# Kernel optimization log

Measured on AMD Instinct MI355X. Metric: run time of the kernel, lower is better.

The kernel has to match this reference:

```python
import jax, jax.numpy as jnp
import numpy as np

D_MODEL = 1024
D_FF = 4096
NUM_EXPERTS = 8
TOP_K = 2
LN_EPS = 1e-5


def setup_inputs() -> dict:
    key = jax.random.key(0)
    ks = jax.random.split(key, 12)
    B, S, D, F, E = 4, 2048, D_MODEL, D_FF, NUM_EXPERTS
    s = 0.02
    return {
        "x": jax.random.normal(ks[0], (B, S, D), jnp.float32),
        # gating network: Linear(D, D//2) -> ReLU -> Linear(D//2, E)
        "gw1": jax.random.normal(ks[1], (D, D // 2), jnp.float32) * s,
        "gb1": jnp.zeros((D // 2,), jnp.float32),
        "gw2": jax.random.normal(ks[2], (D // 2, E), jnp.float32) * s,
        "gb2": jnp.zeros((E,), jnp.float32),
        # stacked expert FFNs: Linear(D,F) -> GELU -> Linear(F,D), then *scale + bias
        "we1": jax.random.normal(ks[3], (E, D, F), jnp.float32) * s,
        "be1": jnp.zeros((E, F), jnp.float32),
        "we2": jax.random.normal(ks[4], (E, F, D), jnp.float32) * s,
        "be2": jnp.zeros((E, D), jnp.float32),
        "escale": jnp.ones((E, D), jnp.float32),
        "ebias": jax.random.normal(ks[5], (E, D), jnp.float32) * 0.01,
        # output LayerNorm
        "gamma": jnp.ones((D,), jnp.float32),
        "beta": jnp.zeros((D,), jnp.float32),
    }


def _layernorm(x, gamma, beta):
    mu = jnp.mean(x, axis=-1, keepdims=True)
    var = jnp.mean(jnp.square(x - mu), axis=-1, keepdims=True)
    return (x - mu) * jax.lax.rsqrt(var + LN_EPS) * gamma + beta


def reference(x, gw1, gb1, gw2, gb2, we1, be1, we2, be2, escale, ebias, gamma, beta):
    B, S, D = x.shape
    xf = x.reshape(-1, D)  # [T, D]

    # ---- gating (eval mode: no noise, no dropout) ----
    gate_logits = jax.nn.relu(xf @ gw1 + gb1) @ gw2 + gb2  # [T, E]
    top_v, top_i = jax.lax.top_k(gate_logits, TOP_K)       # [T, K]
    gates = jax.nn.softmax(top_v, axis=-1)                 # [T, K]

    # load balancing loss: KL( uniform || mean softmax probs ), sum reduction
    probs = jax.nn.softmax(gate_logits, axis=-1)
    expert_probs = probs.mean(axis=0)                      # [E]
    t = 1.0 / NUM_EXPERTS
    load_loss = jnp.sum(t * (jnp.log(t) - jnp.log(expert_probs + 1e-8)))

    # ---- dense compute over ALL experts (faithful to source) ----
    h = jnp.einsum('td,edf->tef', xf, we1) + be1           # [T, E, F]
    h = jax.nn.gelu(h, approximate=False)                  # nn.GELU default = erf
    eo = jnp.einsum('tef,efd->ted', h, we2) + be2          # [T, E, D]
    eo = eo * escale + ebias                               # per-expert scale/bias

    # ---- top-k gather + weighted combine ----
    sel = jnp.take_along_axis(eo, top_i[:, :, None], axis=1)  # [T, K, D]
    out = jnp.sum(gates[:, :, None] * sel, axis=1)            # [T, D]

    y = _layernorm(x + out.reshape(B, S, D), gamma, beta)
    return y, load_loss
```

## Files before the change

### kernel.cpp

```cpp
#include <hip/hip_runtime.h>
#include <hip/hip_bf16.h>
#include <math.h>

#define T_TOK 8192
#define DM    1024
#define DFF   4096
#define NE    8
#define DH    512
#define NSLOT (T_TOK*2)
#define MAXT  136

typedef float  f32x4  __attribute__((ext_vector_type(4)));
typedef __bf16 bf16x8 __attribute__((ext_vector_type(8)));

__device__ inline ushort f2bf(float f) {
  union { float f; unsigned int u; } v; v.f = f;
  unsigned int r = (v.u + 0x7FFFu + ((v.u >> 16) & 1u)) >> 16;
  return (ushort)r;
}

__device__ inline float bf2f(ushort u) {
  union { unsigned int i; float f; } v; v.i = ((unsigned int)u) << 16; return v.f;
}

__device__ __forceinline__ float gelu_erf(float v) {
  float xx = v * 0.70710678118654752f;
  float ax = fabsf(xx);
  float t  = __builtin_amdgcn_rcpf(1.f + 0.3275911f * ax);
  float p  = t * (0.254829592f + t * (-0.284496736f + t * (1.421413741f +
             t * (-1.453152027f + t * 1.061405429f))));
  float er = 1.f - p * __expf(-ax * ax);
  er = copysignf(er, xx);
  return 0.5f * v * (1.f + er);
}

__device__ inline void gl_lds16(const void* g, void* l) {
  __builtin_amdgcn_global_load_lds(
      (const __attribute__((address_space(1))) unsigned int*)g,
      (__attribute__((address_space(3))) unsigned int*)l, 16, 0, 0);
}

__global__ void k_init(int* counts, int* fill, float* psum) {
  int i = threadIdx.x;
  if (i < NE) { counts[i] = 0; fill[i] = 0; psum[i] = 0.f; }
}

__global__ void k_cvt_x(const float* __restrict__ x, ushort* __restrict__ xh,
                        ushort* __restrict__ xl, int n4) {
  int i = blockIdx.x * blockDim.x + threadIdx.x;
  int st = gridDim.x * blockDim.x;
  for (; i < n4; i += st) {
    float4 v = ((const float4*)x)[i];
    ushort4 h, l;
    h.x = f2bf(v.x); l.x = f2bf(v.x - bf2f(h.x));
    h.y = f2bf(v.y); l.y = f2bf(v.y - bf2f(h.y));
    h.z = f2bf(v.z); l.z = f2bf(v.z - bf2f(h.z));
    h.w = f2bf(v.w); l.w = f2bf(v.w - bf2f(h.w));
    ((ushort4*)xh)[i] = h;
    ((ushort4*)xl)[i] = l;
  }
}

__global__ __launch_bounds__(256) void k_tr(const float* __restrict__ in,
                                            ushort* __restrict__ out, int R, int C) {
  __shared__ float tile[64][65];
  int e = blockIdx.z;
  in  += (size_t)e * R * C;
  out += (size_t)e * R * C;
  int r0 = blockIdx.y * 64, c0 = blockIdx.x * 64;
  int tx = threadIdx.x & 63, ty = threadIdx.x >> 6;
  for (int i = 0; i < 16; i++) {
    int r = ty + i * 4;
    tile[r][tx] = in[(size_t)(r0 + r) * C + c0 + tx];
  }
  __syncthreads();
  for (int i = 0; i < 16; i++) {
    int c = ty + i * 4;
    out[(size_t)(c0 + c) * R + r0 + tx] = f2bf(tile[tx][c]);
  }
}

__global__ __launch_bounds__(256) void k_trg(const float* __restrict__ in,
                                             ushort* __restrict__ outh,
                                             ushort* __restrict__ outl) {
  __shared__ float tile[64][65];
  int r0 = blockIdx.y * 64, c0 = blockIdx.x * 64;
  int tx = threadIdx.x & 63, ty = threadIdx.x >> 6;
  for (int i = 0; i < 16; i++) {
    int r = ty + i * 4;
    tile[r][tx] = in[(size_t)(r0 + r) * DH + c0 + tx];
  }
  __syncthreads();
  for (int i = 0; i < 16; i++) {
    int c = ty + i * 4;
    float f = tile[tx][c];
    ushort h = f2bf(f);
    outh[(size_t)(c0 + c) * DM + r0 + tx] = h;
    outl[(size_t)(c0 + c) * DM + r0 + tx] = f2bf(f - bf2f(h));
  }
}

__global__ __launch_bounds__(256) void k_gate1m(const ushort* __restrict__ xh,
                                                const ushort* __restrict__ xl,
                                                const ushort* __restrict__ w1ht,
                                                const ushort* __restrict__ w1lt,
                                                const float* __restrict__ b,
                                                float* __restrict__ g1) {
  constexpr int GX = DH / 128;
  constexpr int NWG = GX * (T_TOK / 128);
  int id = blockIdx.y * GX + blockIdx.x;
  int wg = (id & 7) * (NWG / 8) + (id >> 3);
  int m0 = (wg / GX) * 128;
  int n0 = (wg % GX) * 128;

  __shared__ ushort lds[2][16384];

  int t = threadIdx.x;
  int wave = t >> 6, lane = t & 63;
  int wr = wave >> 1, wc = wave & 1;

  int r = t >> 2;
  int csrc = (((t & 3) ^ ((t >> 3) & 3)) * 8);
  const ushort* ah0 = xh + (size_t)(m0 + r) * DM + csrc;
  const ushort* ah1 = xh + (size_t)(m0 + r + 64) * DM + csrc;
  const ushort* al0 = xl + (size_t)(m0 + r) * DM + csrc;
  const ushort* al1 = xl + (size_t)(m0 + r + 64) * DM + csrc;
  const ushort* bh0 = w1ht + (size_t)(n0 + r) * DM + csrc;
  const ushort* bh1 = w1ht + (size_t)(n0 + r + 64) * DM + csrc;
  const ushort* bl0 = w1lt + (size_t)(n0 + r) * DM + csrc;
  const ushort* bl1 = w1lt + (size_t)(n0 + r + 64) * DM + csrc;

  auto stage = [&](int b_, int k0) {
    ushort* base = lds[b_];
    gl_lds16(ah0 + k0, base + t * 8);
    gl_lds16(ah1 + k0, base + (t + 256) * 8);
    gl_lds16(al0 + k0, base + 4096 + t * 8);
    gl_lds16(al1 + k0, base + 4096 + (t + 256) * 8);
    gl_lds16(bh0 + k0, base + 8192 + t * 8);
    gl_lds16(bh1 + k0, base + 8192 + (t + 256) * 8);
    gl_lds16(bl0 + k0, base + 12288 + t * 8);
    gl_lds16(bl1 + k0, base + 12288 + (t + 256) * 8);
  };

  f32x4 acc[4][4] = {};
  int la = lane & 15;
  int kqs = (((lane >> 4) ^ ((la >> 1) & 3)) * 8);
  constexpr int NT = DM / 32;

  stage(0, 0);
  stage(1, 32);
  for (int kt = 0; kt < NT; kt++) {
    if (kt + 1 < NT) asm volatile("s_waitcnt vmcnt(8)" ::: "memory");
    else             asm volatile("s_waitcnt vmcnt(0)" ::: "memory");
    __builtin_amdgcn_s_barrier();
    const ushort* bb = lds[kt & 1];
    bf16x8 fah[4], fal[4], fbh[4], fbl[4];
#pragma unroll
    for (int m = 0; m < 4; m++) {
      int ro = (wr * 64 + m * 16 + la) * 32 + kqs;
      fah[m] = *(const bf16x8*)&bb[ro];
      fal[m] = *(const bf16x8*)&bb[4096 + ro];
    }
#pragma unroll
    for (int n = 0; n < 4; n++) {
      int ro = (wc * 64 + n * 16 + la) * 32 + kqs;
      fbh[n] = *(const bf16x8*)&bb[8192 + ro];
      fbl[n] = *(const bf16x8*)&bb[12288 + ro];
    }
    asm volatile("s_waitcnt lgkmcnt(0)" ::: "memory");
    __builtin_amdgcn_s_barrier();
    if (kt + 2 < NT) stage(kt & 1, (kt + 2) * 32);
#pragma unroll
    for (int m = 0; m < 4; m++)
#pragma unroll
      for (int n = 0; n < 4; n++)
        acc[m][n] = __builtin_amdgcn_mfma_f32_16x16x32_bf16(fah[m], fbh[n], acc[m][n], 0, 0, 0);
#pragma unroll
    for (int m = 0; m < 4; m++)
#pragma unroll
      for (int n = 0; n < 4; n++)
        acc[m][n] = __builtin_amdgcn_mfma_f32_16x16x32_bf16(fah[m], fbl[n], acc[m][n], 0, 0, 0);
#pragma unroll
    for (int m = 0; m < 4; m++)
#pragma unroll
      for (int n = 0; n < 4; n++)
        acc[m][n] = __builtin_amdgcn_mfma_f32_16x16x32_bf16(fal[m], fbh[n], acc[m][n], 0, 0, 0);
  }

#pragma unroll
  for (int m = 0; m < 4; m++) {
    int rbase = m0 + wr * 64 + m * 16 + ((lane >> 4) << 2);
#pragma unroll
    for (int n = 0; n < 4; n++) {
      int c = n0 + wc * 64 + n * 16 + la;
      float bv = b[c];
      f32x4 a = acc[m][n];
#pragma unroll
      for (int j = 0; j < 4; j++)
        g1[(size_t)(rbase + j) * DH + c] = fmaxf(a[j] + bv, 0.f);
    }
  }
}

__global__ __launch_bounds__(256) void k_gate2(const float* __restrict__ g1,
                                               const float* __restrict__ w2,
                                               const float* __restrict__ b2,
                                               float* __restrict__ logits) {
  int wave = threadIdx.x >> 6, lane = threadIdx.x & 63;
  int tok = blockIdx.x * 4 + wave;
  const float* row = &g1[(size_t)tok * DH];
  float v[8];
#pragma unroll
  for (int j = 0; j < 8; j++) v[j] = row[lane + 64 * j];
  float acc[8];
#pragma unroll
  for (int e = 0; e < NE; e++) {
    float s = 0.f;
#pragma unroll
    for (int j = 0; j < 8; j++) s += v[j] * w2[(size_t)(lane + 64 * j) * NE + e];
    acc[e] = s;
  }
  for (int off = 32; off > 0; off >>= 1)
#pragma unroll
    for (int e = 0; e < NE; e++) acc[e] += __shfl_down(acc[e], off);
  if (lane == 0)
#pragma unroll
    for (int e = 0; e < NE; e++) logits[(size_t)tok * NE + e] = acc[e] + b2[e];
}

__global__ __launch_bounds__(256) void k_route(const float* __restrict__ logits,
                                               int* __restrict__ topi,
                                               float* __restrict__ gatesw,
                                               int* __restrict__ counts,
                                               float* __restrict__ psum) {
  int t = blockIdx.x * blockDim.x + threadIdx.x;
  const float* lp = &logits[(size_t)t * NE];
  float l[8];
#pragma unroll
  for (int e = 0; e < NE; e++) l[e] = lp[e];
  int i0 = 0; float v0 = l[0];
#pragma unroll
  for (int e = 1; e < NE; e++) if (l[e] > v0) { v0 = l[e]; i0 = e; }
  int i1 = (i0 == 0) ? 1 : 0; float v1 = l[i1];
#pragma unroll
  for (int e = 0; e < NE; e++)
    if (e != i0 && l[e] > v1) { v1 = l[e]; i1 = e; }
  float g0 = 1.f / (1.f + expf(v1 - v0));
  topi[t * 2] = i0; topi[t * 2 + 1] = i1;
  gatesw[t * 2] = g0; gatesw[t * 2 + 1] = 1.f - g0;
  float p[8]; float s = 0.f;
#pragma unroll
  for (int e = 0; e < NE; e++) { p[e] = expf(l[e] - v0); s += p[e]; }
  float inv = 1.f / s;
  int lane = threadIdx.x & 63;
#pragma unroll
  for (int e = 0; e < NE; e++) {
    float pe = p[e] * inv;
    for (int off = 32; off > 0; off >>= 1) pe += __shfl_down(pe, off);
    if (lane == 0) atomicAdd(&psum[e], pe);
  }
#pragma unroll
  for (int e = 0; e < NE; e++) {
    unsigned long long m0 = __ballot(i0 == e);
    unsigned long long m1 = __ballot(i1 == e);
    if (lane == 0) {
      int c = __popcll(m0) + __popcll(m1);
      if (c) atomicAdd(&counts[e], c);
    }
  }
}

__global__ void k_scan(const int* __restrict__ counts, int* __restrict__ offsets,
                       const float* __restrict__ psum, float* __restrict__ loss_out,
                       int* __restrict__ tile_e, int* __restrict__ tile_mt) {
  if (threadIdx.x == 0) {
    int off = 0;
    for (int e = 0; e < NE; e++) { offsets[e] = off; off += counts[e]; }
    offsets[NE] = off;
    float tt = 1.f / NE, loss = 0.f;
    for (int e = 0; e < NE; e++) {
      float pe = psum[e] / (float)T_TOK;
      loss += tt * (logf(tt) - logf(pe + 1e-8f));
    }
    loss_out[0] = loss;
    int n = 0;
    for (int e = 0; e < NE; e++) {
      int rows = counts[e];
      for (int mt = 0; mt * 128 < rows; mt++) { tile_e[n] = e; tile_mt[n] = mt; n++; }
    }
    for (int i = n; i < MAXT; i++) { tile_e[i] = -1; tile_mt[i] = 0; }
  }
}

__global__ __launch_bounds__(256) void k_fill(const int* __restrict__ topi,
                                              const int* __restrict__ offsets,
                                              int* __restrict__ fill,
                                              int* __restrict__ slot_tok,
                                              int* __restrict__ tok_slot) {
  int t = blockIdx.x * blockDim.x + threadIdx.x;
  for (int k = 0; k < 2; k++) {
    int e = topi[t * 2 + k];
    int pos = offsets[e] + atomicAdd(&fill[e], 1);
    slot_tok[pos] = t;
    tok_slot[t * 2 + k] = pos;
  }
}

__global__ __launch_bounds__(256, 3) void k_egemm1(const ushort* __restrict__ xb,
                                                   const ushort* __restrict__ w1t,
                                                   const float* __restrict__ be1,
                                                   const int* __restrict__ slot_tok,
                                                   const int* __restrict__ offsets,
                                                   const int* __restrict__ tile_e,
                                                   const int* __restrict__ tile_mt,
                                                   ushort* __restrict__ H) {
  constexpr int GX = DFF / 128;
  constexpr int NWG = GX * MAXT;
  int id = blockIdx.y * GX + blockIdx.x;
  int wg = (id & 7) * (NWG / 8) + (id >> 3);
  int ty = wg / GX;
  int n0 = (wg % GX) * 128;
  int e = tile_e[ty];
  if (e < 0) return;
  int mt = tile_mt[ty];
  int beg = offsets[e], nrows = offsets[e + 1] - beg;
  const ushort* B = w1t + (size_t)e * DFF * DM;

  __shared__ ushort As[2][4096];
  __shared__ ushort Bs[2][4096];

  int t = threadIdx.x;
  int wave = t >> 6, lane = t & 63;
  int wr = wave >> 1, wc = wave & 1;

  int r_g0 = mt * 128 + (t >> 2);
  int r_g1 = r_g0 + 64;
  int tok0 = slot_tok[beg + (r_g0 < nrows ? r_g0 : 0)];
  int tok1 = slot_tok[beg + (r_g1 < nrows ? r_g1 : 0)];
  int acol = (((t & 3) ^ ((t >> 3) & 3)) * 8);
  const ushort* aptr0 = xb + (size_t)tok0 * DM + acol;
  const ushort* aptr1 = xb + (size_t)tok1 * DM + acol;
  const ushort* bptr0 = B + (size_t)(n0 + (t >> 2)) * DM + acol;
  const ushort* bptr1 = B + (size_t)(n0 + (t >> 2) + 64) * DM + acol;
  char* adst = (char*)As + t * 16;
  char* bdst = (char*)Bs + t * 16;

  auto stage = [&](int b, int k0) {
    gl_lds16(aptr0 + k0, adst + b * 8192);
    gl_lds16(aptr1 + k0, adst + b * 8192 + 4096);
    gl_lds16(bptr0 + k0, bdst + b * 8192);
    gl_lds16(bptr1 + k0, bdst + b * 8192 + 4096);
  };

  f32x4 acc[4][4] = {};
  int la = lane & 15;
  int kqs = (((lane >> 4) ^ ((la >> 1) & 3)) * 8);
  constexpr int NT = DM / 32;

  stage(0, 0);
  stage(1, 32);
  for (int kt = 0; kt < NT; kt++) {
    if (kt + 1 < NT) asm volatile("s_waitcnt vmcnt(4)" ::: "memory");
    else             asm volatile("s_waitcnt vmcnt(0)" ::: "memory");
    __builtin_amdgcn_s_barrier();
    const ushort* Ab = As[kt & 1];
    const ushort* Bb = Bs[kt & 1];
    bf16x8 af[4], bfr[4];
#pragma unroll
    for (int m = 0; m < 4; m++)
      af[m] = *(const bf16x8*)&Ab[(wr * 64 + m * 16 + la) * 32 + kqs];
#pragma unroll
    for (int n = 0; n < 4; n++)
      bfr[n] = *(const bf16x8*)&Bb[(wc * 64 + n * 16 + la) * 32 + kqs];
    asm volatile("s_waitcnt lgkmcnt(0)" ::: "memory");
    __builtin_amdgcn_s_barrier();
    if (kt + 2 < NT) stage(kt & 1, (kt + 2) * 32);
#pragma unroll
    for (int m = 0; m < 4; m++)
#pragma unroll
      for (int n = 0; n < 4; n++)
        acc[m][n] = __builtin_amdgcn_mfma_f32_16x16x32_bf16(af[m], bfr[n], acc[m][n], 0, 0, 0);
  }

  int row0 = mt * 128 + wr * 64;
  int c_of = n0 + wc * 64;
#pragma unroll
  for (int m = 0; m < 4; m++) {
    int rbase = row0 + m * 16 + ((lane >> 4) << 2);
#pragma unroll
    for (int n = 0; n < 4; n++) {
      int c = c_of + n * 16 + la;
      float b1 = be1[e * DFF + c];
      f32x4 a = acc[m][n];
#pragma unroll
      for (int j = 0; j < 4; j++) {
        int rr = rbase + j;
        if (rr < nrows) {
          float v = a[j] + b1;
          H[(size_t)(beg + rr) * DFF + c] = f2bf(gelu_erf(v));
        }
      }
    }
  }
}

__global__ __launch_bounds__(256, 3) void k_egemm2(const ushort* __restrict__ H,
                                                   const ushort* __restrict__ w2t,
                                                   const float* __restrict__ be2,
                                                   const float* __restrict__ escale,
                                                   const float* __restrict__ ebias,
                                                   const int* __restrict__ offsets,
                                                   const int* __restrict__ tile_e,
                                                   const int* __restrict__ tile_mt,
                                                   ushort* __restrict__ eo) {
  constexpr int GX = DM / 128;
  constexpr int NWG = GX * MAXT;
  int id = blockIdx.y * GX + blockIdx.x;
  int wg = (id & 7) * (NWG / 8) + (id >> 3);
  int ty = wg / GX;
  int n0 = (wg % GX) * 128;
  int e = tile_e[ty];
  if (e < 0) return;
  int mt = tile_mt[ty];
  int beg = offsets[e], nrows = offsets[e + 1] - beg;
  const ushort* B = w2t + (size_t)e * DM * DFF;

  __shared__ ushort As[2][4096];
  __shared__ ushort Bs[2][4096];

  int t = threadIdx.x;
  int wave = t >> 6, lane = t & 63;
  int wr = wave >> 1, wc = wave & 1;

  int r_g0 = mt * 128 + (t >> 2);
  int r_g1 = r_g0 + 64;
  int s0 = beg + (r_g0 < nrows ? r_g0 : 0);
  int s1 = beg + (r_g1 < nrows ? r_g1 : 0);
  int acol = (((t & 3) ^ ((t >> 3) & 3)) * 8);
  const ushort* aptr0 = H + (size_t)s0 * DFF + acol;
  const ushort* aptr1 = H + (size_t)s1 * DFF + acol;
  const ushort* bptr0 = B + (size_t)(n0 + (t >> 2)) * DFF + acol;
  const ushort* bptr1 = B + (size_t)(n0 + (t >> 2) + 64) * DFF + acol;
  char* adst = (char*)As + t * 16;
  char* bdst = (char*)Bs + t * 16;

  auto stage = [&](int b, int k0) {
    gl_lds16(aptr0 + k0, adst + b * 8192);
    gl_lds16(aptr1 + k0, adst + b * 8192 + 4096);
    gl_lds16(bptr0 + k0, bdst + b * 8192);
    gl_lds16(bptr1 + k0, bdst + b * 8192 + 4096);
  };

  f32x4 acc[4][4] = {};
  int la = lane & 15;
  int kqs = (((lane >> 4) ^ ((la >> 1) & 3)) * 8);
  constexpr int NT = DFF / 32;

  stage(0, 0);
  stage(1, 32);
  for (int kt = 0; kt < NT; kt++) {
    if (kt + 1 < NT) asm volatile("s_waitcnt vmcnt(4)" ::: "memory");
    else             asm volatile("s_waitcnt vmcnt(0)" ::: "memory");
    __builtin_amdgcn_s_barrier();
    const ushort* Ab = As[kt & 1];
    const ushort* Bb = Bs[kt & 1];
    bf16x8 af[4], bfr[4];
#pragma unroll
    for (int m = 0; m < 4; m++)
      af[m] = *(const bf16x8*)&Ab[(wr * 64 + m * 16 + la) * 32 + kqs];
#pragma unroll
    for (int n = 0; n < 4; n++)
      bfr[n] = *(const bf16x8*)&Bb[(wc * 64 + n * 16 + la) * 32 + kqs];
    asm volatile("s_waitcnt lgkmcnt(0)" ::: "memory");
    __builtin_amdgcn_s_barrier();
    if (kt + 2 < NT) stage(kt & 1, (kt + 2) * 32);
#pragma unroll
    for (int m = 0; m < 4; m++)
#pragma unroll
      for (int n = 0; n < 4; n++)
        acc[m][n] = __builtin_amdgcn_mfma_f32_16x16x32_bf16(af[m], bfr[n], acc[m][n], 0, 0, 0);
  }

  int row0 = mt * 128 + wr * 64;
  int c_of = n0 + wc * 64;
#pragma unroll
  for (int m = 0; m < 4; m++) {
    int rbase = row0 + m * 16 + ((lane >> 4) << 2);
#pragma unroll
    for (int n = 0; n < 4; n++) {
      int c = c_of + n * 16 + la;
      float b2 = be2[e * DM + c];
      float sc = escale[e * DM + c];
      float bb = ebias[e * DM + c];
      f32x4 a = acc[m][n];
#pragma unroll
      for (int j = 0; j < 4; j++) {
        int rr = rbase + j;
        if (rr < nrows) {
          float v = (a[j] + b2) * sc + bb;
          eo[(size_t)(beg + rr) * DM + c] = f2bf(v);
        }
      }
    }
  }
}

__global__ __launch_bounds__(256) void k_ln(const float* __restrict__ x,
                                            const ushort* __restrict__ eo,
                                            const int* __restrict__ tok_slot,
                                            const float* __restrict__ gatesw,
                                            const float* __restrict__ gamma,
                                            const float* __restrict__ beta,
                                            float* __restrict__ y) {
  int t = blockIdx.x;
  int s0 = tok_slot[t * 2], s1 = tok_slot[t * 2 + 1];
  float g0 = gatesw[t * 2], g1 = gatesw[t * 2 + 1];
  const float* xr = &x[(size_t)t * DM];
  const ushort* e0 = &eo[(size_t)s0 * DM];
  const ushort* e1 = &eo[(size_t)s1 * DM];
  int tid = threadIdx.x;
  int c0 = tid * 4;
  float4 xv = *(const float4*)&xr[c0];
  ushort4 a0 = *(const ushort4*)&e0[c0];
  ushort4 a1 = *(const ushort4*)&e1[c0];
  float v[4];
  v[0] = xv.x + g0 * bf2f(a0.x) + g1 * bf2f(a1.x);
  v[1] = xv.y + g0 * bf2f(a0.y) + g1 * bf2f(a1.y);
  v[2] = xv.z + g0 * bf2f(a0.z) + g1 * bf2f(a1.z);
  v[3] = xv.w + g0 * bf2f(a0.w) + g1 * bf2f(a1.w);
  float sum = v[0] + v[1] + v[2] + v[3];
  __shared__ float red[4];
  __shared__ float red2[4];
  for (int off = 32; off > 0; off >>= 1) sum += __shfl_down(sum, off);
  if ((tid & 63) == 0) red[tid >> 6] = sum;
  __syncthreads();
  float mu = (red[0] + red[1] + red[2] + red[3]) * (1.f / DM);
  float vs = 0.f;
#pragma unroll
  for (int i = 0; i < 4; i++) { float d = v[i] - mu; vs += d * d; }
  for (int off = 32; off > 0; off >>= 1) vs += __shfl_down(vs, off);
  if ((tid & 63) == 0) red2[tid >> 6] = vs;
  __syncthreads();
  float var = (red2[0] + red2[1] + red2[2] + red2[3]) * (1.f / DM);
  float rs = rsqrtf(var + 1e-5f);
  float4 gm = *(const float4*)&gamma[c0];
  float4 bt = *(const float4*)&beta[c0];
  float4 o;
  o.x = (v[0] - mu) * rs * gm.x + bt.x;
  o.y = (v[1] - mu) * rs * gm.y + bt.y;
  o.z = (v[2] - mu) * rs * gm.z + bt.z;
  o.w = (v[3] - mu) * rs * gm.w + bt.w;
  *(float4*)&y[(size_t)t * DM + c0] = o;
}

extern "C" void kernel_launch(void* const* d_in, const int* in_sizes, int n_in,
                              void* d_out, int out_size, void* d_ws, size_t ws_size,
                              hipStream_t stream) {
  const float* x    = (const float*)d_in[0];
  const float* gw1  = (const float*)d_in[1];
  const float* gb1  = (const float*)d_in[2];
  const float* gw2  = (const float*)d_in[3];
  const float* gb2  = (const float*)d_in[4];
  const float* we1  = (const float*)d_in[5];
  const float* be1  = (const float*)d_in[6];
  const float* we2  = (const float*)d_in[7];
  const float* be2  = (const float*)d_in[8];
  const float* escale = (const float*)d_in[9];
  const float* ebias  = (const float*)d_in[10];
  const float* gamma  = (const float*)d_in[11];
  const float* beta   = (const float*)d_in[12];
  float* y = (float*)d_out;
  float* loss_out = y + (size_t)T_TOK * DM;

  char* w = (char*)d_ws;
  ushort* xh    = (ushort*)w; w += (size_t)T_TOK * DM * 2;
  ushort* xl    = (ushort*)w; w += (size_t)T_TOK * DM * 2;
  ushort* w1t   = (ushort*)w; w += (size_t)NE * DFF * DM * 2;
  ushort* w2t   = (ushort*)w; w += (size_t)NE * DM * DFF * 2;
  ushort* H     = (ushort*)w; w += (size_t)NSLOT * DFF * 2;
  ushort* eo    = (ushort*)w; w += (size_t)NSLOT * DM * 2;
  ushort* w1ht  = (ushort*)w; w += (size_t)DH * DM * 2;
  ushort* w1lt  = (ushort*)w; w += (size_t)DH * DM * 2;
  float* g1     = (float*)w;  w += (size_t)T_TOK * DH * 4;
  float* logits = (float*)w;  w += (size_t)T_TOK * NE * 4;
  int*   topi   = (int*)w;    w += (size_t)T_TOK * 2 * 4;
  float* gatesw = (float*)w;  w += (size_t)T_TOK * 2 * 4;
  int* slot_tok = (int*)w;    w += (size_t)NSLOT * 4;
  int* tok_slot = (int*)w;    w += (size_t)T_TOK * 2 * 4;
  int* counts   = (int*)w;    w += 64;
  int* fill     = (int*)w;    w += 64;
  int* offsets  = (int*)w;    w += 64;
  float* psum   = (float*)w;  w += 64;
  int* tile_e   = (int*)w;    w += MAXT * 4 + 32;
  int* tile_mt  = (int*)w;    w += MAXT * 4 + 32;

  k_init<<<1, 64, 0, stream>>>(counts, fill, psum);
  k_cvt_x<<<2048, 256, 0, stream>>>(x, xh, xl, T_TOK * DM / 4);
  k_trg<<<dim3(8, 16), 256, 0, stream>>>(gw1, w1ht, w1lt);
  k_tr<<<dim3(64, 16, 8), 256, 0, stream>>>(we1, w1t, DM, DFF);
  k_tr<<<dim3(16, 64, 8), 256, 0, stream>>>(we2, w2t, DFF, DM);
  k_gate1m<<<dim3(DH / 128, T_TOK / 128), 256, 0, stream>>>(xh, xl, w1ht, w1lt, gb1, g1);
  k_gate2<<<T_TOK / 4, 256, 0, stream>>>(g1, gw2, gb2, logits);
  k_route<<<T_TOK / 256, 256, 0, stream>>>(logits, topi, gatesw, counts, psum);
  k_scan<<<1, 64, 0, stream>>>(counts, offsets, psum, loss_out, tile_e, tile_mt);
  k_fill<<<T_TOK / 256, 256, 0, stream>>>(topi, offsets, fill, slot_tok, tok_slot);
  k_egemm1<<<dim3(DFF / 128, MAXT), 256, 0, stream>>>(xh, w1t, be1, slot_tok, offsets,
                                                      tile_e, tile_mt, H);
  k_egemm2<<<dim3(DM / 128, MAXT), 256, 0, stream>>>(H, w2t, be2, escale, ebias,
                                                     offsets, tile_e, tile_mt, eo);
  k_ln<<<T_TOK, 256, 0, stream>>>(x, eo, tok_slot, gatesw, gamma, beta, y);
}
```

Measured before the change: 688.8 us.

## Enlarge expert GEMM tiles to 256x256 with 8-wave phased LDS pipeline

Both expert GEMMs move from 128x128 tiles with 4 waves and K-step 32 to 256x256 tiles with 8 waves and K-step 64, using a 128KB LDS buffer. The main loop is split into phases that interleave global-to-LDS staging of the next K slice with MFMA quads, and raises wave priority around the MFMA blocks. The aim is more operand reuse per byte loaded and better overlap of memory with compute. In exchange, larger tiles waste more padded rows on the per-expert remainder tiles, fewer workgroups are launched, and the larger LDS footprint lowers occupancy.

```diff
diff --git a/kernel.cpp b/kernel.cpp
--- a/kernel.cpp
+++ b/kernel.cpp
@@ -8,7 +8,7 @@
 #define NE    8
 #define DH    512
 #define NSLOT (T_TOK*2)
-#define MAXT  136
+#define MAXT2 72
 
 typedef float  f32x4  __attribute__((ext_vector_type(4)));
 typedef __bf16 bf16x8 __attribute__((ext_vector_type(8)));
@@ -39,6 +39,12 @@
       (const __attribute__((address_space(1))) unsigned int*)g,
       (__attribute__((address_space(3))) unsigned int*)l, 16, 0, 0);
 }
+
+#define SBAR   __builtin_amdgcn_s_barrier()
+#define SCHEDB __builtin_amdgcn_sched_barrier(0)
+#define LGKM0  asm volatile("s_waitcnt lgkmcnt(0)" ::: "memory")
+#define LGKM8  asm volatile("s_waitcnt lgkmcnt(8)" ::: "memory")
+#define VM4    asm volatile("s_waitcnt vmcnt(4)" ::: "memory")
 
 __global__ void k_init(int* counts, int* fill, float* psum) {
   int i = threadIdx.x;
@@ -286,9 +292,9 @@
     int n = 0;
     for (int e = 0; e < NE; e++) {
       int rows = counts[e];
-      for (int mt = 0; mt * 128 < rows; mt++) { tile_e[n] = e; tile_mt[n] = mt; n++; }
-    }
-    for (int i = n; i < MAXT; i++) { tile_e[i] = -1; tile_mt[i] = 0; }
+      for (int mt = 0; mt * 256 < rows; mt++) { tile_e[n] = e; tile_mt[n] = mt; n++; }
+    }
+    for (int i = n; i < MAXT2; i++) { tile_e[i] = -1; tile_mt[i] = 0; }
   }
 }
 
@@ -306,7 +312,35 @@
   }
 }
 
-__global__ __launch_bounds__(256, 3) void k_egemm1(const ushort* __restrict__ xb,
+#define STG1(BUF, OH, P0, P1, KT) do { \
+    gl_lds16((P0) + (size_t)(KT) * 64, ld0 + (BUF) * 32768 + (OH) * 8192); \
+    gl_lds16((P1) + (size_t)(KT) * 64, ld0 + (BUF) * 32768 + (OH) * 8192 + 4096); } while (0)
+#define RD_A(BUFP, MB) do { _Pragma("unroll") \
+    for (int m_ = 0; m_ < 4; m_++) { \
+      af[m_][0] = *(const bf16x8*)((BUFP) + Abase + ((MB) + m_) * 1024 + pk0); \
+      af[m_][1] = *(const bf16x8*)((BUFP) + Abase + ((MB) + m_) * 1024 + pk1); } } while (0)
+#define RD_B(BUFP, NB, D) do { _Pragma("unroll") \
+    for (int n_ = 0; n_ < 2; n_++) { \
+      D[n_][0] = *(const bf16x8*)((BUFP) + Bbase + ((NB) + n_) * 1024 + pk0); \
+      D[n_][1] = *(const bf16x8*)((BUFP) + Bbase + ((NB) + n_) * 1024 + pk1); } } while (0)
+#define QUAD(MB, NB, D) do { _Pragma("unroll") \
+    for (int m_ = 0; m_ < 4; m_++) { _Pragma("unroll") \
+      for (int n_ = 0; n_ < 2; n_++) { \
+        acc[(MB)+m_][(NB)+n_] = __builtin_amdgcn_mfma_f32_16x16x32_bf16(af[m_][0], D[n_][0], acc[(MB)+m_][(NB)+n_], 0, 0, 0); \
+        acc[(MB)+m_][(NB)+n_] = __builtin_amdgcn_mfma_f32_16x16x32_bf16(af[m_][1], D[n_][1], acc[(MB)+m_][(NB)+n_], 0, 0, 0); } } } while (0)
+
+#define PHASE_RD(BUF, BUFP, RDSTMT, STG_STMT, MB, NB, D, BIGRD) do { \
+    RDSTMT; STG_STMT; \
+    if (BIGRD) { LGKM8; } \
+    SBAR; LGKM0; SCHEDB; \
+    __builtin_amdgcn_s_setprio(1); QUAD(MB, NB, D); __builtin_amdgcn_s_setprio(0); \
+    SBAR; } while (0)
+#define PHASE_NORD(STG_STMT, MB, NB, D) do { \
+    STG_STMT; SBAR; SCHEDB; \
+    __builtin_amdgcn_s_setprio(1); QUAD(MB, NB, D); __builtin_amdgcn_s_setprio(0); \
+    VM4; SBAR; } while (0)
+
+__global__ __launch_bounds__(512, 2) void k_egemm1(const ushort* __restrict__ xb,
                                                    const ushort* __restrict__ w1t,
                                                    const float* __restrict__ be1,
                                                    const int* __restrict__ slot_tok,
@@ -314,97 +348,92 @@
                                                    const int* __restrict__ tile_e,
                                                    const int* __restrict__ tile_mt,
                                                    ushort* __restrict__ H) {
-  constexpr int GX = DFF / 128;
-  constexpr int NWG = GX * MAXT;
+  constexpr int GX = DFF / 256;
+  constexpr int NWG = GX * MAXT2;
+  constexpr int NT = DM / 64;
   int id = blockIdx.y * GX + blockIdx.x;
   int wg = (id & 7) * (NWG / 8) + (id >> 3);
   int ty = wg / GX;
-  int n0 = (wg % GX) * 128;
+  int n0c = (wg % GX) * 256;
   int e = tile_e[ty];
   if (e < 0) return;
   int mt = tile_mt[ty];
   int beg = offsets[e], nrows = offsets[e + 1] - beg;
-  const ushort* B = w1t + (size_t)e * DFF * DM;
-
-  __shared__ ushort As[2][4096];
-  __shared__ ushort Bs[2][4096];
+  const ushort* Bw = w1t + (size_t)e * DFF * DM;
+
+  __shared__ ushort lds[65536];
 
   int t = threadIdx.x;
-  int wave = t >> 6, lane = t & 63;
-  int wr = wave >> 1, wc = wave & 1;
-
-  int r_g0 = mt * 128 + (t >> 2);
-  int r_g1 = r_g0 + 64;
-  int tok0 = slot_tok[beg + (r_g0 < nrows ? r_g0 : 0)];
-  int tok1 = slot_tok[beg + (r_g1 < nrows ? r_g1 : 0)];
-  int acol = (((t & 3) ^ ((t >> 3) & 3)) * 8);
-  const ushort* aptr0 = xb + (size_t)tok0 * DM + acol;
-  const ushort* aptr1 = xb + (size_t)tok1 * DM + acol;
-  const ushort* bptr0 = B + (size_t)(n0 + (t >> 2)) * DM + acol;
-  const ushort* bptr1 = B + (size_t)(n0 + (t >> 2) + 64) * DM + acol;
-  char* adst = (char*)As + t * 16;
-  char* bdst = (char*)Bs + t * 16;
-
-  auto stage = [&](int b, int k0) {
-    gl_lds16(aptr0 + k0, adst + b * 8192);
-    gl_lds16(aptr1 + k0, adst + b * 8192 + 4096);
-    gl_lds16(bptr0 + k0, bdst + b * 8192);
-    gl_lds16(bptr1 + k0, bdst + b * 8192 + 4096);
+  int lane = t & 63, la = lane & 15, lh = lane >> 4;
+  int wid = t >> 6, wm = wid >> 2, wn = wid & 3;
+
+  int tr = t >> 3;
+  int cX = ((t & 7) ^ (tr & 7)) * 8;
+  auto arow = [&](int r) {
+    r = mt * 256 + r; if (r >= nrows) r = nrows - 1;
+    return (size_t)slot_tok[beg + r];
   };
-
-  f32x4 acc[4][4] = {};
-  int la = lane & 15;
-  int kqs = (((lane >> 4) ^ ((la >> 1) & 3)) * 8);
-  constexpr int NT = DM / 32;
-
-  stage(0, 0);
-  stage(1, 32);
-  for (int kt = 0; kt < NT; kt++) {
-    if (kt + 1 < NT) asm volatile("s_waitcnt vmcnt(4)" ::: "memory");
-    else             asm volatile("s_waitcnt vmcnt(0)" ::: "memory");
-    __builtin_amdgcn_s_barrier();
-    const ushort* Ab = As[kt & 1];
-    const ushort* Bb = Bs[kt & 1];
-    bf16x8 af[4], bfr[4];
-#pragma unroll
-    for (int m = 0; m < 4; m++)
-      af[m] = *(const bf16x8*)&Ab[(wr * 64 + m * 16 + la) * 32 + kqs];
-#pragma unroll
-    for (int n = 0; n < 4; n++)
-      bfr[n] = *(const bf16x8*)&Bb[(wc * 64 + n * 16 + la) * 32 + kqs];
-    asm volatile("s_waitcnt lgkmcnt(0)" ::: "memory");
-    __builtin_amdgcn_s_barrier();
-    if (kt + 2 < NT) stage(kt & 1, (kt + 2) * 32);
-#pragma unroll
-    for (int m = 0; m < 4; m++)
-#pragma unroll
-      for (int n = 0; n < 4; n++)
-        acc[m][n] = __builtin_amdgcn_mfma_f32_16x16x32_bf16(af[m], bfr[n], acc[m][n], 0, 0, 0);
-  }
-
-  int row0 = mt * 128 + wr * 64;
-  int c_of = n0 + wc * 64;
-#pragma unroll
-  for (int m = 0; m < 4; m++) {
-    int rbase = row0 + m * 16 + ((lane >> 4) << 2);
+  const ushort* pA00 = xb + arow(tr) * DM + cX;
+  const ushort* pA01 = xb + arow(64 + tr) * DM + cX;
+  const ushort* pA10 = xb + arow(128 + tr) * DM + cX;
+  const ushort* pA11 = xb + arow(192 + tr) * DM + cX;
+  const ushort* pB00 = Bw + (size_t)(n0c + tr) * DM + cX;
+  const ushort* pB01 = Bw + (size_t)(n0c + 64 + tr) * DM + cX;
+  const ushort* pB10 = Bw + (size_t)(n0c + 128 + tr) * DM + cX;
+  const ushort* pB11 = Bw + (size_t)(n0c + 192 + tr) * DM + cX;
+  ushort* ld0 = lds + t * 8;
+
+  int pk0 = (lh ^ (la & 7)) * 8;
+  int pk1 = ((4 + lh) ^ (la & 7)) * 8;
+  int Abase = wm * 8192 + la * 64;
+  int Bbase = 16384 + (wn >> 1) * 8192 + ((wn & 1) * 64 + la) * 64;
+
+  f32x4 acc[8][4] = {};
+  bf16x8 af[4][2], blo[2][2], bhi[2][2];
+
+  STG1(0, 0, pA00, pA01, 0);
+  STG1(0, 1, pA10, pA11, 0);
+  STG1(0, 2, pB00, pB01, 0);
+  STG1(0, 3, pB10, pB11, 0);
+  STG1(1, 2, pB00, pB01, 1);
+  STG1(1, 3, pB10, pB11, 1);
+  VM4; SBAR;
+
+  const ushort* b0p = lds;
+  const ushort* b1p = lds + 32768;
+  for (int it = 0; it < NT / 2; it++) {
+    int t1 = 2 * it + 1;
+    int t2 = (2 * it + 2 < NT) ? 2 * it + 2 : NT - 1;
+    int t3 = (t1 + 2 < NT) ? t1 + 2 : NT - 1;
+    PHASE_RD(1, b0p, { RD_A(b0p, 0); RD_B(b0p, 0, blo); }, STG1(1, 0, pA00, pA01, t1), 0, 0, blo, 1);
+    PHASE_RD(1, b0p, { RD_B(b0p, 2, bhi); },               STG1(1, 1, pA10, pA11, t1), 0, 2, bhi, 0);
+    PHASE_RD(0, b0p, { RD_A(b0p, 4); },                    STG1(0, 2, pB00, pB01, t2), 4, 0, blo, 0);
+    PHASE_NORD(STG1(0, 3, pB10, pB11, t2), 4, 2, bhi);
+    PHASE_RD(0, b1p, { RD_A(b1p, 0); RD_B(b1p, 0, blo); }, STG1(0, 0, pA00, pA01, t2), 0, 0, blo, 1);
+    PHASE_RD(0, b1p, { RD_B(b1p, 2, bhi); },               STG1(0, 1, pA10, pA11, t2), 0, 2, bhi, 0);
+    PHASE_RD(1, b1p, { RD_A(b1p, 4); },                    STG1(1, 2, pB00, pB01, t3), 4, 0, blo, 0);
+    PHASE_NORD(STG1(1, 3, pB10, pB11, t3), 4, 2, bhi);
+  }
+
+#pragma unroll
+  for (int m = 0; m < 8; m++) {
+    int lrow = mt * 256 + wm * 128 + m * 16 + lh * 4;
 #pragma unroll
     for (int n = 0; n < 4; n++) {
-      int c = c_of + n * 16 + la;
+      int c = n0c + wn * 64 + n * 16 + la;
       float b1 = be1[e * DFF + c];
       f32x4 a = acc[m][n];
 #pragma unroll
       for (int j = 0; j < 4; j++) {
-        int rr = rbase + j;
-        if (rr < nrows) {
-          float v = a[j] + b1;
-          H[(size_t)(beg + rr) * DFF + c] = f2bf(gelu_erf(v));
-        }
+        int rr = lrow + j;
+        if (rr < nrows)
+          H[(size_t)(beg + rr) * DFF + c] = f2bf(gelu_erf(a[j] + b1));
       }
     }
   }
 }
 
-__global__ __launch_bounds__(256, 3) void k_egemm2(const ushort* __restrict__ H,
+__global__ __launch_bounds__(512, 2) void k_egemm2(const ushort* __restrict__ H,
                                                    const ushort* __restrict__ w2t,
                                                    const float* __restrict__ be2,
                                                    const float* __restrict__ escale,
@@ -413,93 +442,88 @@
                                                    const int* __restrict__ tile_e,
                                                    const int* __restrict__ tile_mt,
                                                    ushort* __restrict__ eo) {
-  constexpr int GX = DM / 128;
-  constexpr int NWG = GX * MAXT;
+  constexpr int GX = DM / 256;
+  constexpr int NWG = GX * MAXT2;
+  constexpr int NT = DFF / 64;
   int id = blockIdx.y * GX + blockIdx.x;
   int wg = (id & 7) * (NWG / 8) + (id >> 3);
   int ty = wg / GX;
-  int n0 = (wg % GX) * 128;
+  int n0c = (wg % GX) * 256;
   int e = tile_e[ty];
   if (e < 0) return;
   int mt = tile_mt[ty];
   int beg = offsets[e], nrows = offsets[e + 1] - beg;
-  const ushort* B = w2t + (size_t)e * DM * DFF;
-
-  __shared__ ushort As[2][4096];
-  __shared__ ushort Bs[2][4096];
+  const ushort* Bw = w2t + (size_t)e * DM * DFF;
+
+  __shared__ ushort lds[65536];
 
   int t = threadIdx.x;
-  int wave = t >> 6, lane = t & 63;
-  int wr = wave >> 1, wc = wave & 1;
-
-  int r_g0 = mt * 128 + (t >> 2);
-  int r_g1 = r_g0 + 64;
-  int s0 = beg + (r_g0 < nrows ? r_g0 : 0);
-  int s1 = beg + (r_g1 < nrows ? r_g1 : 0);
-  int acol = (((t & 3) ^ ((t >> 3) & 3)) * 8);
-  const ushort* aptr0 = H + (size_t)s0 * DFF + acol;
-  const ushort* aptr1 = H + (size_t)s1 * DFF + acol;
-  const ushort* bptr0 = B + (size_t)(n0 + (t >> 2)) * DFF + acol;
-  const ushort* bptr1 = B + (size_t)(n0 + (t >> 2) + 64) * DFF + acol;
-  char* adst = (char*)As + t * 16;
-  char* bdst = (char*)Bs + t * 16;
-
-  auto stage = [&](int b, int k0) {
-    gl_lds16(aptr0 + k0, adst + b * 8192);
-    gl_lds16(aptr1 + k0, adst + b * 8192 + 4096);
-    gl_lds16(bptr0 + k0, bdst + b * 8192);
-    gl_lds16(bptr1 + k0, bdst + b * 8192 + 4096);
+  int lane = t & 63, la = lane & 15, lh = lane >> 4;
+  int wid = t >> 6, wm = wid >> 2, wn = wid & 3;
+
+  int tr = t >> 3;
+  int cX = ((t & 7) ^ (tr & 7)) * 8;
+  auto arow = [&](int r) {
+    r = mt * 256 + r; if (r >= nrows) r = nrows - 1;
+    return (size_t)(beg + r);
   };
-
-  f32x4 acc[4][4] = {};
-  int la = lane & 15;
-  int kqs = (((lane >> 4) ^ ((la >> 1) & 3)) * 8);
-  constexpr int NT = DFF / 32;
-
-  stage(0, 0);
-  stage(1, 32);
-  for (int kt = 0; kt < NT; kt++) {
-    if (kt + 1 < NT) asm volatile("s_waitcnt vmcnt(4)" ::: "memory");
-    else             asm volatile("s_waitcnt vmcnt(0)" ::: "memory");
-    __builtin_amdgcn_s_barrier();
-    const ushort* Ab = As[kt & 1];
-    const ushort* Bb = Bs[kt & 1];
-    bf16x8 af[4], bfr[4];
-#pragma unroll
-    for (int m = 0; m < 4; m++)
-      af[m] = *(const bf16x8*)&Ab[(wr * 64 + m * 16 + la) * 32 + kqs];
-#pragma unroll
-    for (int n = 0; n < 4; n++)
-      bfr[n] = *(const bf16x8*)&Bb[(wc * 64 + n * 16 + la) * 32 + kqs];
-    asm volatile("s_waitcnt lgkmcnt(0)" ::: "memory");
-    __builtin_amdgcn_s_barrier();
-    if (kt + 2 < NT) stage(kt & 1, (kt + 2) * 32);
-#pragma unroll
-    for (int m = 0; m < 4; m++)
-#pragma unroll
-      for (int n = 0; n < 4; n++)
-        acc[m][n] = __builtin_amdgcn_mfma_f32_16x16x32_bf16(af[m], bfr[n], acc[m][n], 0, 0, 0);
-  }
-
-  int row0 = mt * 128 + wr * 64;
-  int c_of = n0 + wc * 64;
-#pragma unroll
-  for (int m = 0; m < 4; m++) {
-    int rbase = row0 + m * 16 + ((lane >> 4) << 2);
+  const ushort* pA00 = H + arow(tr) * DFF + cX;
+  const ushort* pA01 = H + arow(64 + tr) * DFF + cX;
+  const ushort* pA10 = H + arow(128 + tr) * DFF + cX;
+  const ushort* pA11 = H + arow(192 + tr) * DFF + cX;
+  const ushort* pB00 = Bw + (size_t)(n0c + tr) * DFF + cX;
+  const ushort* pB01 = Bw + (size_t)(n0c + 64 + tr) * DFF + cX;
+  const ushort* pB10 = Bw + (size_t)(n0c + 128 + tr) * DFF + cX;
+  const ushort* pB11 = Bw + (size_t)(n0c + 192 + tr) * DFF + cX;
+  ushort* ld0 = lds + t * 8;
+
+  int pk0 = (lh ^ (la & 7)) * 8;
+  int pk1 = ((4 + lh) ^ (la & 7)) * 8;
+  int Abase = wm * 8192 + la * 64;
+  int Bbase = 16384 + (wn >> 1) * 8192 + ((wn & 1) * 64 + la) * 64;
+
+  f32x4 acc[8][4] = {};
+  bf16x8 af[4][2], blo[2][2], bhi[2][2];
+
+  STG1(0, 0, pA00, pA01, 0);
+  STG1(0, 1, pA10, pA11, 0);
+  STG1(0, 2, pB00, pB01, 0);
+  STG1(0, 3, pB10, pB11, 0);
+  STG1(1, 2, pB00, pB01, 1);
+  STG1(1, 3, pB10, pB11, 1);
+  VM4; SBAR;
+
+  const ushort* b0p = lds;
+  const ushort* b1p = lds + 32768;
+  for (int it = 0; it < NT / 2; it++) {
+    int t1 = 2 * it + 1;
+    int t2 = (2 * it + 2 < NT) ? 2 * it + 2 : NT - 1;
+    int t3 = (t1 + 2 < NT) ? t1 + 2 : NT - 1;
+    PHASE_RD(1, b0p, { RD_A(b0p, 0); RD_B(b0p, 0, blo); }, STG1(1, 0, pA00, pA01, t1), 0, 0, blo, 1);
+    PHASE_RD(1, b0p, { RD_B(b0p, 2, bhi); },               STG1(1, 1, pA10, pA11, t1), 0, 2, bhi, 0);
+    PHASE_RD(0, b0p, { RD_A(b0p, 4); },                    STG1(0, 2, pB00, pB01, t2), 4, 0, blo, 0);
+    PHASE_NORD(STG1(0, 3, pB10, pB11, t2), 4, 2, bhi);
+    PHASE_RD(0, b1p, { RD_A(b1p, 0); RD_B(b1p, 0, blo); }, STG1(0, 0, pA00, pA01, t2), 0, 0, blo, 1);
+    PHASE_RD(0, b1p, { RD_B(b1p, 2, bhi); },               STG1(0, 1, pA10, pA11, t2), 0, 2, bhi, 0);
+    PHASE_RD(1, b1p, { RD_A(b1p, 4); },                    STG1(1, 2, pB00, pB01, t3), 4, 0, blo, 0);
+    PHASE_NORD(STG1(1, 3, pB10, pB11, t3), 4, 2, bhi);
+  }
+
+#pragma unroll
+  for (int m = 0; m < 8; m++) {
+    int lrow = mt * 256 + wm * 128 + m * 16 + lh * 4;
 #pragma unroll
     for (int n = 0; n < 4; n++) {
-      int c = c_of + n * 16 + la;
+      int c = n0c + wn * 64 + n * 16 + la;
       float b2 = be2[e * DM + c];
       float sc = escale[e * DM + c];
       float bb = ebias[e * DM + c];
       f32x4 a = acc[m][n];
 #pragma unroll
       for (int j = 0; j < 4; j++) {
-        int rr = rbase + j;
-        if (rr < nrows) {
-          float v = (a[j] + b2) * sc + bb;
-          eo[(size_t)(beg + rr) * DM + c] = f2bf(v);
-        }
+        int rr = lrow + j;
+        if (rr < nrows)
+          eo[(size_t)(beg + rr) * DM + c] = f2bf((a[j] + b2) * sc + bb);
       }
     }
   }
@@ -591,8 +615,8 @@
   int* fill     = (int*)w;    w += 64;
   int* offsets  = (int*)w;    w += 64;
   float* psum   = (float*)w;  w += 64;
-  int* tile_e   = (int*)w;    w += MAXT * 4 + 32;
-  int* tile_mt  = (int*)w;    w += MAXT * 4 + 32;
+  int* tile_e   = (int*)w;    w += MAXT2 * 4 + 32;
+  int* tile_mt  = (int*)w;    w += MAXT2 * 4 + 32;
 
   k_init<<<1, 64, 0, stream>>>(counts, fill, psum);
   k_cvt_x<<<2048, 256, 0, stream>>>(x, xh, xl, T_TOK * DM / 4);
@@ -604,9 +628,9 @@
   k_route<<<T_TOK / 256, 256, 0, stream>>>(logits, topi, gatesw, counts, psum);
   k_scan<<<1, 64, 0, stream>>>(counts, offsets, psum, loss_out, tile_e, tile_mt);
   k_fill<<<T_TOK / 256, 256, 0, stream>>>(topi, offsets, fill, slot_tok, tok_slot);
-  k_egemm1<<<dim3(DFF / 128, MAXT), 256, 0, stream>>>(xh, w1t, be1, slot_tok, offsets,
-                                                      tile_e, tile_mt, H);
-  k_egemm2<<<dim3(DM / 128, MAXT), 256, 0, stream>>>(H, w2t, be2, escale, ebias,
-                                                     offsets, tile_e, tile_mt, eo);
+  k_egemm1<<<dim3(DFF / 256, MAXT2), 512, 0, stream>>>(xh, w1t, be1, slot_tok, offsets,
+                                                       tile_e, tile_mt, H);
+  k_egemm2<<<dim3(DM / 256, MAXT2), 512, 0, stream>>>(H, w2t, be2, escale, ebias,
+                                                      offsets, tile_e, tile_mt, eo);
   k_ln<<<T_TOK, 256, 0, stream>>>(x, eo, tok_slot, gatesw, gamma, beta, y);
 }
```

Result: slower. 743.8 us (+8.0%).
